# Performance work log

Hardware: AMD Instinct MI355X
Metric: run time of the kernel (lower is better)

The kernel has to match this reference:

```python
import jax, jax.numpy as jnp
import numpy as np

N, E, F_IN, HID, H, NCLS, L = 100000, 1600000, 128, 128, 4, 40, 2
C = HID // H  # per-head channels = 32
LN_EPS = 1e-5
SOFTMAX_EPS = 1e-16  # PyG softmax denominator epsilon


def setup_inputs() -> dict:
    key = jax.random.key(0)
    ks = jax.random.split(key, 8)
    s = 1.0 / np.sqrt(F_IN).astype(np.float32)
    return {
        "x": jax.random.normal(ks[0], (N, F_IN), jnp.float32),
        "edge_index": jax.random.randint(ks[1], (2, E), 0, N, jnp.int32),
        "Wq": jax.random.normal(ks[2], (L, F_IN, HID), jnp.float32) * s,
        "bq": jnp.zeros((L, HID), jnp.float32),
        "Wk": jax.random.normal(ks[3], (L, F_IN, HID), jnp.float32) * s,
        "bk": jnp.zeros((L, HID), jnp.float32),
        "Wv": jax.random.normal(ks[4], (L, F_IN, HID), jnp.float32) * s,
        "bv": jnp.zeros((L, HID), jnp.float32),
        "Ws": jax.random.normal(ks[5], (L, F_IN, HID), jnp.float32) * s,
        "bs": jnp.zeros((L, HID), jnp.float32),
        "gamma": jnp.ones((L, HID), jnp.float32),
        "beta": jnp.zeros((L, HID), jnp.float32),
        "Wout": jax.random.normal(ks[6], (HID, NCLS), jnp.float32) * (1.0 / np.sqrt(HID).astype(np.float32)),
        "bout": jnp.zeros((NCLS,), jnp.float32),
    }


def _transformer_conv(x, src, dst, Wq, bq, Wk, bk, Wv, bv, Ws, bs):
    # PyG TransformerConv, concat=False, root_weight=True, beta=False
    n = x.shape[0]
    q = (x @ Wq + bq).reshape(n, H, C)
    k = (x @ Wk + bk).reshape(n, H, C)
    v = (x @ Wv + bv).reshape(n, H, C)
    # per-edge attention logits: [E, H]
    alpha = jnp.einsum('ehc,ehc->eh', q[dst], k[src]) / np.sqrt(C).astype(np.float32)
    # segment softmax over incoming edges of each destination node
    amax = jax.ops.segment_max(alpha, dst, num_segments=n)        # [N, H]
    ex = jnp.exp(alpha - amax[dst])                               # [E, H]
    denom = jax.ops.segment_sum(ex, dst, num_segments=n)         # [N, H]
    w = ex / (denom[dst] + SOFTMAX_EPS)                           # [E, H]
    msg = v[src] * w[:, :, None]                                  # [E, H, C]
    out = jax.ops.segment_sum(msg, dst, num_segments=n)          # [N, H, C]
    out = out.mean(axis=1)                                        # concat=False -> head average, [N, C*?]. Here C*H==HID only via mean over H of C dims -> [N, C]
    # NOTE: concat=False averages heads -> [N, C]; skip proj maps in->C? In PyG, out_channels=hidden here,
    # so lin_* are Linear(in, heads*hidden)... but TransformerConv(in, hidden) means out_channels=hidden/?
    return out


def _conv(x, src, dst, Wq, bq, Wk, bk, Wv, bv, Ws, bs):
    # Faithful version with out_channels = HID per head? No: TransformerConv(in, hidden, heads, concat=False)
    # in PyG uses out_channels=hidden and lin_* : in -> heads*out_channels. To keep HID total width we model
    # per-head dim C = HID // H (standard multi-head factorization with same total width HID).
    n = x.shape[0]
    q = (x @ Wq + bq).reshape(n, H, C)
    k = (x @ Wk + bk).reshape(n, H, C)
    v = (x @ Wv + bv).reshape(n, H, C)
    alpha = jnp.einsum('ehc,ehc->eh', q[dst], k[src]) / np.sqrt(C).astype(np.float32)
    amax = jax.ops.segment_max(alpha, dst, num_segments=n)
    ex = jnp.exp(alpha - amax[dst])
    denom = jax.ops.segment_sum(ex, dst, num_segments=n)
    w = ex / (denom[dst] + SOFTMAX_EPS)
    msg = (v[src] * w[:, :, None]).reshape(-1, H * C)             # [E, HID]
    agg = jax.ops.segment_sum(msg, dst, num_segments=n)          # [N, HID]
    # concat=False -> mean over heads, then broadcast back is not what PyG does; PyG yields [N, out_channels].
    out = agg.reshape(n, H, C).mean(axis=1)                       # [N, C]
    out = jnp.tile(out, (1, H))                                   # widen back to HID? No — instead use skip of width HID.
    return out


def _conv_layer(x, src, dst, Wq, bq, Wk, bk, Wv, bv, Ws, bs):
    """TransformerConv(in, HID, heads=H, concat=False): lin_{q,k,v}: in -> H*HID is too wide for a
    memory target, so we use the equivalent standard factorization HID = H*C (per-head C), giving
    attention output [N, H, C]; concat=False head-mean is applied per head group and the result is
    projected residually via lin_skip (in -> HID)."""
    n = x.shape[0]
    q = (x @ Wq + bq).reshape(n, H, C)
    k = (x @ Wk + bk).reshape(n, H, C)
    v = (x @ Wv + bv).reshape(n, H, C)
    alpha = jnp.einsum('ehc,ehc->eh', q[dst], k[src]) / np.sqrt(C).astype(np.float32)
    amax = jax.ops.segment_max(alpha, dst, num_segments=n)        # [N, H]
    ex = jnp.exp(alpha - amax[dst])                               # [E, H]
    denom = jax.ops.segment_sum(ex, dst, num_segments=n)
    w = ex / (denom[dst] + SOFTMAX_EPS)
    msg = (v[src] * w[:, :, None]).reshape(-1, HID)               # [E, HID] (head-concat)
    agg = jax.ops.segment_sum(msg, dst, num_segments=n)          # [N, HID]
    return agg + x @ Ws + bs                                      # root/skip connection


def _layernorm(h, g, b):
    mu = h.mean(-1, keepdims=True)
    var = ((h - mu) ** 2).mean(-1, keepdims=True)
    return (h - mu) * jax.lax.rsqrt(var + LN_EPS) * g + b


def reference(x, edge_index, Wq, bq, Wk, bk, Wv, bv, Ws, bs, gamma, beta, Wout, bout):
    src, dst = edge_index[0], edge_index[1]
    h = x
    for l in range(L):  # fixed small layer count
        h = _conv_layer(h, src, dst, Wq[l], bq[l], Wk[l], bk[l], Wv[l], bv[l], Ws[l], bs[l])
        h = jax.nn.relu(_layernorm(h, gamma[l], beta[l]))
        # dropout is identity in eval mode
    return h @ Wout + bout  # [N, NCLS]
```

## Files before the change

kernel.cpp:

```cpp
#include <hip/hip_runtime.h>
#include <math.h>

#define N_NODES 100000
#define N_EDGES 1600000
#define NCLS_ 40
#define NSCAN_BLOCKS ((N_NODES + 1023) / 1024)
#define DRANGE 12500
#define SRCS_PAD (N_EDGES + 3 * N_NODES + 64)

#define QSCALE (0.17677669529663687f * 1.4426950408889634f)

#if __has_builtin(__builtin_amdgcn_exp2f)
#define EXP2(x) __builtin_amdgcn_exp2f(x)
#else
#define EXP2(x) exp2f(x)
#endif

typedef short bf16x8 __attribute__((ext_vector_type(8)));
typedef float f32x4 __attribute__((ext_vector_type(4)));

__device__ __forceinline__ unsigned short f2b(float f) {
    union { float f; unsigned u; } v; v.f = f;
    unsigned r = v.u + 0x7fffu + ((v.u >> 16) & 1u);
    return (unsigned short)(r >> 16);
}
__device__ __forceinline__ float2 up2(unsigned u) {
    union { unsigned u; float f; } a, b;
    a.u = u << 16; b.u = u & 0xffff0000u;
    return make_float2(a.f, b.f);
}
__device__ __forceinline__ unsigned pk2(float x, float y) {
    return (unsigned)f2b(x) | ((unsigned)f2b(y) << 16);
}
__device__ __forceinline__ float b2f(unsigned short s) {
    union { unsigned u; float f; } v; v.u = ((unsigned)s) << 16;
    return v.f;
}


__global__ void zero_i32_kernel(int* __restrict__ p, int n) {
    int i = blockIdx.x * blockDim.x + threadIdx.x;
    if (i < n) p[i] = 0;
}

__global__ __launch_bounds__(256) void wconv_kernel(
    const float* __restrict__ Wq, const float* __restrict__ Wk,
    const float* __restrict__ Wv, const float* __restrict__ Ws,
    unsigned short* __restrict__ Wbf) {
    int tid = blockIdx.x * 256 + threadIdx.x;
    if (tid >= 131072) return;
    int k   = tid & 127;
    int n   = (tid >> 7) & 63;
    int g   = (tid >> 13) & 1;
    int mat = (tid >> 14) & 3;
    int l   = tid >> 16;
    const float* W = (mat == 0) ? Wq : (mat == 1) ? Wk : (mat == 2) ? Wv : Ws;
    float w = W[l * 16384 + k * 128 + g * 64 + n];
    if (mat == 0) w *= QSCALE;
    Wbf[tid] = f2b(w);
}

__global__ __launch_bounds__(256) void hist_kernel(
    const int* __restrict__ dst, int* __restrict__ deg) {
    int group = blockIdx.x & 7;
    int gblk  = blockIdx.x >> 3;
    int nblk  = gridDim.x >> 3;
    int lo = group * DRANGE, hi = lo + DRANGE;
    for (int i = gblk * 256 + threadIdx.x; i < N_EDGES; i += nblk * 256) {
        int d = dst[i];
        if (d >= lo && d < hi) atomicAdd(&deg[d], 1);
    }
}

__global__ __launch_bounds__(1024) void scan_block_kernel(
    const int* __restrict__ deg, int* __restrict__ rowptr, int* __restrict__ sums) {
    __shared__ int tmp[1024];
    int t = threadIdx.x;
    int i = blockIdx.x * 1024 + t;
    int v = (i < N_NODES) ? ((deg[i] + 3) & ~3) : 0;
    tmp[t] = v;
    __syncthreads();
    for (int d = 1; d < 1024; d <<= 1) {
        int add = (t >= d) ? tmp[t - d] : 0;
        __syncthreads();
        tmp[t] += add;
        __syncthreads();
    }
    if (i < N_NODES) rowptr[i] = tmp[t] - v;
    if (t == 1023) sums[blockIdx.x] = tmp[1023];
}

__global__ __launch_bounds__(128) void scan_sums_kernel(int* __restrict__ sums) {
    __shared__ int tmp[128];
    int t = threadIdx.x;
    int v = (t < NSCAN_BLOCKS) ? sums[t] : 0;
    tmp[t] = v;
    __syncthreads();
    for (int d = 1; d < 128; d <<= 1) {
        int add = (t >= d) ? tmp[t - d] : 0;
        __syncthreads();
        tmp[t] += add;
        __syncthreads();
    }
    if (t < NSCAN_BLOCKS) sums[t] = tmp[t] - v;
}

__global__ void scan_add_kernel(int* __restrict__ rowptr, const int* __restrict__ sums,
                                int* __restrict__ cursor) {
    int i = blockIdx.x * blockDim.x + threadIdx.x;
    if (i < N_NODES) {
        int val = rowptr[i] + sums[i >> 10];
        rowptr[i] = val;
        cursor[i] = val;
    }
}

__global__ __launch_bounds__(256) void scatter_kernel(
    const int* __restrict__ src, const int* __restrict__ dst,
    int* __restrict__ cursor, int* __restrict__ srcs) {
    int group = blockIdx.x & 7;
    int gblk  = blockIdx.x >> 3;
    int nblk  = gridDim.x >> 3;
    int lo = group * DRANGE, hi = lo + DRANGE;
    for (int i = gblk * 256 + threadIdx.x; i < N_EDGES; i += nblk * 256) {
        int d = dst[i];
        if (d >= lo && d < hi) {
            int pos = atomicAdd(&cursor[d], 1);
            srcs[pos] = src[i] << 10;
        }
    }
}

__global__ __launch_bounds__(256) void gemm_qkvs_kernel(
    const void* __restrict__ Ap, int a_is_bf16,
    const unsigned short* __restrict__ Wbf,
    const float* __restrict__ b0, const float* __restrict__ b1,
    const float* __restrict__ b2, const float* __restrict__ b3,
    unsigned short* __restrict__ out) {
    __shared__ unsigned short As[64][138];
    __shared__ unsigned short Bs[2][64][138];
    int t = threadIdx.x;
    int row0 = blockIdx.x * 64;

    if (a_is_bf16) {
        const unsigned short* A = (const unsigned short*)Ap;
        for (int i = 0; i < 8; ++i) {
            int idx = t + i * 256;
            int r = idx >> 5, k4 = (idx & 31) << 2;
            ushort4 v = make_ushort4(0, 0, 0, 0);
            if (row0 + r < N_NODES) v = *(const ushort4*)&A[(size_t)(row0 + r) * 128 + k4];
            *(ushort4*)&As[r][k4] = v;
        }
    } else {
        const float* A = (const float*)Ap;
        for (int i = 0; i < 8; ++i) {
            int idx = t + i * 256;
            int r = idx >> 5, k4 = (idx & 31) << 2;
            float4 v = make_float4(0.f, 0.f, 0.f, 0.f);
            if (row0 + r < N_NODES) v = *(const float4*)&A[(size_t)(row0 + r) * 128 + k4];
            ushort4 o;
            o.x = f2b(v.x); o.y = f2b(v.y); o.z = f2b(v.z); o.w = f2b(v.w);
            *(ushort4*)&As[r][k4] = o;
        }
    }

    int wv = t >> 6, lane = t & 63;
    int ln = lane & 15, quad = lane >> 4;

    ushort4 pf[8];
    {
        const unsigned short* Wg = Wbf;
        for (int i = 0; i < 8; ++i) {
            int idx = t + i * 256;
            pf[i] = *(const ushort4*)&Wg[((idx >> 5) << 7) + ((idx & 31) << 2)];
        }
        for (int i = 0; i < 8; ++i) {
            int idx = t + i * 256;
            *(ushort4*)&Bs[0][idx >> 5][(idx & 31) << 2] = pf[i];
        }
    }
    __syncthreads();

    #pragma unroll
    for (int g = 0; g < 8; ++g) {
        int mat = g >> 1;
        int cur = g & 1;
        const float* bias = (mat == 0) ? b0 : (mat == 1) ? b1 : (mat == 2) ? b2 : b3;
        int cb = (g & 1) * 64;

        if (g < 7) {
            const unsigned short* Wg = Wbf + (size_t)(g + 1) * 8192;
            for (int i = 0; i < 8; ++i) {
                int idx = t + i * 256;
                pf[i] = *(const ushort4*)&Wg[((idx >> 5) << 7) + ((idx & 31) << 2)];
            }
        }

        f32x4 acc[4];
        for (int c = 0; c < 4; ++c) acc[c] = (f32x4){0.f, 0.f, 0.f, 0.f};
        for (int ks = 0; ks < 4; ++ks) {
            int k0 = ks * 32 + quad * 8;
            bf16x8 x = *(bf16x8*)&As[wv * 16 + ln][k0];
            for (int c = 0; c < 4; ++c) {
                bf16x8 w = *(bf16x8*)&Bs[cur][c * 16 + ln][k0];
                acc[c] = __builtin_amdgcn_mfma_f32_16x16x32_bf16(w, x, acc[c], 0, 0, 0);
            }
        }

        int node = row0 + wv * 16 + ln;
        bool ok = node < N_NODES;
        for (int c = 0; c < 4; ++c) {
            int ch = cb + c * 16 + quad * 4;
            float4 bb = *(const float4*)&bias[ch];
            float s = (mat == 0) ? QSCALE : 1.0f;
            float v0 = acc[c][0] + bb.x * s;
            float v1 = acc[c][1] + bb.y * s;
            float v2 = acc[c][2] + bb.z * s;
            float v3 = acc[c][3] + bb.w * s;
            int pos;
            if (mat == 0)      pos = ch;
            else if (mat == 3) pos = 384 + ch;
            else               pos = 128 + (ch << 1) + ((mat == 2) ? 4 : 0);
            if (ok) {
                uint2 wd;
                wd.x = pk2(v0, v1);
                wd.y = pk2(v2, v3);
                *(uint2*)&out[(size_t)node * 512 + pos] = wd;
            }
        }

        if (g < 7) {
            int nxt = cur ^ 1;
            for (int i = 0; i < 8; ++i) {
                int idx = t + i * 256;
                *(ushort4*)&Bs[nxt][idx >> 5][(idx & 31) << 2] = pf[i];
            }
        }
        __syncthreads();
    }
}

#define EDGE(KV, ECOND) {                                            \
        float2 k01 = up2(KV.x), k23 = up2(KV.y);                     \
        float p = q01.x*k01.x + q01.y*k01.y + q23.x*k23.x + q23.y*k23.y; \
        p += __shfl_xor(p, 1);                                       \
        p += __shfl_xor(p, 2);                                       \
        p += __shfl_xor(p, 4);                                       \
        float e = (ECOND);                                           \
        float2 v01 = up2(KV.z), v23 = up2(KV.w);                     \
        a0 = fmaf(e, v01.x, a0); a1 = fmaf(e, v01.y, a1);            \
        a2 = fmaf(e, v23.x, a2); a3 = fmaf(e, v23.y, a3);            \
        dsum += e; }

__global__ __launch_bounds__(256) void edge_fused_kernel(
    const unsigned short* __restrict__ qkvs,
    const int* __restrict__ srcs, const int* __restrict__ rowptr,
    const int* __restrict__ deg,
    const float* __restrict__ gamma, const float* __restrict__ beta,
    unsigned short* __restrict__ hout) {
    int n = (blockIdx.x * 256 + threadIdx.x) >> 6;
    int lane = threadIdx.x & 63;
    if (n >= N_NODES) return;
    int half = lane >> 5, hl = lane & 31;
    const unsigned short* qrow = qkvs + (size_t)n * 512;
    uint2 qu = *(const uint2*)&qrow[4 * hl];
    float2 q01 = up2(qu.x), q23 = up2(qu.y);
    uint2 su = *(const uint2*)&qrow[384 + 4 * hl];
    float2 sk01 = up2(su.x), sk23 = up2(su.y);
    int e0 = rowptr[n];
    int rem = deg[n];
    const char* kbase = (const char*)qkvs + 256 + 16 * hl;
    const int* sb = srcs + e0 + 4 * half;
    float a0 = 0.f, a1 = 0.f, a2 = 0.f, a3 = 0.f, dsum = 0.f;

    int4 oc;
    if (rem >= 8) oc = *(const int4*)sb;
    while (rem >= 8) {
        int4 on;
        if (rem >= 16) on = *(const int4*)(sb + 8);
        uint4 kv0 = *(const uint4*)(kbase + (unsigned)oc.x);
        uint4 kv1 = *(const uint4*)(kbase + (unsigned)oc.y);
        uint4 kv2 = *(const uint4*)(kbase + (unsigned)oc.z);
        uint4 kv3 = *(const uint4*)(kbase + (unsigned)oc.w);
        EDGE(kv0, EXP2(p));
        EDGE(kv1, EXP2(p));
        EDGE(kv2, EXP2(p));
        EDGE(kv3, EXP2(p));
        oc = on; sb += 8; rem -= 8;
    }
    if (rem > 0) {
        int4 ot = *(const int4*)sb;
        int tb = 4 * half;
        uint4 kv0 = *(const uint4*)(kbase + (unsigned)ot.x);
        uint4 kv1 = *(const uint4*)(kbase + (unsigned)ot.y);
        uint4 kv2 = *(const uint4*)(kbase + (unsigned)ot.z);
        uint4 kv3 = *(const uint4*)(kbase + (unsigned)ot.w);
        EDGE(kv0, (tb + 0 < rem) ? EXP2(p) : 0.f);
        EDGE(kv1, (tb + 1 < rem) ? EXP2(p) : 0.f);
        EDGE(kv2, (tb + 2 < rem) ? EXP2(p) : 0.f);
        EDGE(kv3, (tb + 3 < rem) ? EXP2(p) : 0.f);
    }

    a0 += __shfl_xor(a0, 32); a1 += __shfl_xor(a1, 32);
    a2 += __shfl_xor(a2, 32); a3 += __shfl_xor(a3, 32);
    dsum += __shfl_xor(dsum, 32);
    float dinv = 1.0f / (dsum + 1e-16f);
    float o0 = a0 * dinv + sk01.x, o1 = a1 * dinv + sk01.y;
    float o2 = a2 * dinv + sk23.x, o3 = a3 * dinv + sk23.y;
    float sum = o0 + o1 + o2 + o3;
    for (int m = 1; m < 64; m <<= 1) sum += __shfl_xor(sum, m);
    float mu = sum * (1.0f / 256.0f);
    float d0 = o0 - mu, d1 = o1 - mu, d2 = o2 - mu, d3 = o3 - mu;
    float sq = d0 * d0 + d1 * d1 + d2 * d2 + d3 * d3;
    for (int m = 1; m < 64; m <<= 1) sq += __shfl_xor(sq, m);
    float rs = rsqrtf(sq * (1.0f / 256.0f) + 1e-5f);
    if (half == 0) {
        float4 g4 = *(const float4*)&gamma[4 * hl];
        float4 b4 = *(const float4*)&beta[4 * hl];
        float r0 = fmaxf(d0 * rs * g4.x + b4.x, 0.f);
        float r1 = fmaxf(d1 * rs * g4.y + b4.y, 0.f);
        float r2 = fmaxf(d2 * rs * g4.z + b4.z, 0.f);
        float r3 = fmaxf(d3 * rs * g4.w + b4.w, 0.f);
        uint2 w;
        w.x = pk2(r0, r1);
        w.y = pk2(r2, r3);
        *(uint2*)&hout[(size_t)n * 128 + 4 * hl] = w;
    }
}

__global__ __launch_bounds__(256) void out_gemm_kernel(
    const unsigned short* __restrict__ h, const float* __restrict__ Wout,
    const float* __restrict__ bout, float* __restrict__ out) {
    int wv = __builtin_amdgcn_readfirstlane((int)(threadIdx.x >> 6));
    int l = threadIdx.x & 63;
    int n = blockIdx.x * 64 + l;
    int jb = wv * 10;
    int nc = (n < N_NODES) ? n : (N_NODES - 1);
    const unsigned short* hrow = h + (size_t)nc * 128;
    uint4 hp[16];
    #pragma unroll
    for (int i = 0; i < 16; ++i) hp[i] = *(const uint4*)&hrow[i * 8];
    float acc[10];
    #pragma unroll
    for (int j = 0; j < 10; ++j) acc[j] = bout[jb + j];
    #pragma unroll
    for (int i = 0; i < 16; ++i) {
        float2 c01 = up2(hp[i].x), c23 = up2(hp[i].y);
        float2 c45 = up2(hp[i].z), c67 = up2(hp[i].w);
        float hc0 = c01.x, hc1 = c01.y, hc2 = c23.x, hc3 = c23.y;
        float hc4 = c45.x, hc5 = c45.y, hc6 = c67.x, hc7 = c67.y;
        #pragma unroll
        for (int j = 0; j < 10; ++j) {
            const float* wk = Wout + (i * 8) * NCLS_ + jb + j;
            acc[j] = fmaf(hc0, wk[0 * NCLS_], acc[j]);
            acc[j] = fmaf(hc1, wk[1 * NCLS_], acc[j]);
            acc[j] = fmaf(hc2, wk[2 * NCLS_], acc[j]);
            acc[j] = fmaf(hc3, wk[3 * NCLS_], acc[j]);
            acc[j] = fmaf(hc4, wk[4 * NCLS_], acc[j]);
            acc[j] = fmaf(hc5, wk[5 * NCLS_], acc[j]);
            acc[j] = fmaf(hc6, wk[6 * NCLS_], acc[j]);
            acc[j] = fmaf(hc7, wk[7 * NCLS_], acc[j]);
        }
    }
    if (n < N_NODES) {
        #pragma unroll
        for (int j = 0; j < 10; ++j) out[(size_t)n * NCLS_ + jb + j] = acc[j];
    }
}

extern "C" void kernel_launch(void* const* d_in, const int* in_sizes, int n_in,
                              void* d_out, int out_size, void* d_ws, size_t ws_size,
                              hipStream_t stream) {
    const float* x    = (const float*)d_in[0];
    const int*   ei   = (const int*)d_in[1];
    const int*   src  = ei;
    const int*   dst  = ei + N_EDGES;
    const float* Wq   = (const float*)d_in[2];
    const float* bq   = (const float*)d_in[3];
    const float* Wk   = (const float*)d_in[4];
    const float* bk   = (const float*)d_in[5];
    const float* Wv   = (const float*)d_in[6];
    const float* bv   = (const float*)d_in[7];
    const float* Wsk  = (const float*)d_in[8];
    const float* bsk  = (const float*)d_in[9];
    const float* gmm  = (const float*)d_in[10];
    const float* bta  = (const float*)d_in[11];
    const float* Wout = (const float*)d_in[12];
    const float* bout = (const float*)d_in[13];
    float* outp = (float*)d_out;

    char* p = (char*)d_ws;
    auto carve = [&](size_t bytes) {
        char* r = p;
        p += (bytes + 255) & ~(size_t)255;
        return r;
    };
    unsigned short* qkvs = (unsigned short*)carve((size_t)N_NODES * 512 * 2);
    unsigned short* h    = (unsigned short*)carve((size_t)N_NODES * 128 * 2);
    unsigned short* Wbf  = (unsigned short*)carve((size_t)131072 * 2);
    int* deg     = (int*)carve((size_t)N_NODES * 4);
    int* rowptr  = (int*)carve((size_t)(N_NODES + 1) * 4);
    int* cursor  = (int*)carve((size_t)N_NODES * 4);
    int* srcs    = (int*)carve((size_t)SRCS_PAD * 4);
    int* sums    = (int*)carve((size_t)NSCAN_BLOCKS * 4);

    wconv_kernel<<<512, 256, 0, stream>>>(Wq, Wk, Wv, Wsk, Wbf);

    zero_i32_kernel<<<(N_NODES + 255) / 256, 256, 0, stream>>>(deg, N_NODES);
    zero_i32_kernel<<<(SRCS_PAD + 255) / 256, 256, 0, stream>>>(srcs, SRCS_PAD);
    hist_kernel<<<2048, 256, 0, stream>>>(dst, deg);
    scan_block_kernel<<<NSCAN_BLOCKS, 1024, 0, stream>>>(deg, rowptr, sums);
    scan_sums_kernel<<<1, 128, 0, stream>>>(sums);
    scan_add_kernel<<<(N_NODES + 255) / 256, 256, 0, stream>>>(rowptr, sums, cursor);
    scatter_kernel<<<2048, 256, 0, stream>>>(src, dst, cursor, srcs);

    for (int l = 0; l < 2; ++l) {
        const void* hin = l ? (const void*)h : (const void*)x;
        gemm_qkvs_kernel<<<(N_NODES + 63) / 64, 256, 0, stream>>>(
            hin, l, Wbf + (size_t)l * 65536,
            bq + l * 128, bk + l * 128, bv + l * 128, bsk + l * 128, qkvs);
        edge_fused_kernel<<<(N_NODES + 3) / 4, 256, 0, stream>>>(
            qkvs, srcs, rowptr, deg, gmm + l * 128, bta + l * 128, h);
    }
    out_gemm_kernel<<<(N_NODES + 63) / 64, 256, 0, stream>>>(h, Wout, bout, outp);
}
```

Before: 685.4 us.

## Load GEMM A fragments into registers, double block rows, use hardware bf16 pack

The QKVS GEMM now loads each wave's A-row fragments straight from global memory into registers instead of staging them through shared memory. Blocks grow to 512 threads covering 128 rows, so each staged weight tile is reused by twice as many rows. The software round-to-nearest bf16 packing is replaced by the v_cvt_pk_bf16_f32 instruction in the GEMM and the edge kernel. Together these aim to cut LDS traffic, weight reloads per row and conversion ALU work, at the cost of more registers per thread and reliance on the inline-asm instruction's rounding matching the old path.

```diff
diff --git a/kernel.cpp b/kernel.cpp
--- a/kernel.cpp
+++ b/kernel.cpp
@@ -24,13 +24,15 @@
     unsigned r = v.u + 0x7fffu + ((v.u >> 16) & 1u);
     return (unsigned short)(r >> 16);
 }
+__device__ __forceinline__ unsigned cvtpk(float x, float y) {
+    unsigned r;
+    asm("v_cvt_pk_bf16_f32 %0, %1, %2" : "=v"(r) : "v"(x), "v"(y));
+    return r;
+}
 __device__ __forceinline__ float2 up2(unsigned u) {
     union { unsigned u; float f; } a, b;
     a.u = u << 16; b.u = u & 0xffff0000u;
     return make_float2(a.f, b.f);
-}
-__device__ __forceinline__ unsigned pk2(float x, float y) {
-    return (unsigned)f2b(x) | ((unsigned)f2b(y) << 16);
 }
 __device__ __forceinline__ float b2f(unsigned short s) {
     union { unsigned u; float f; } v; v.u = ((unsigned)s) << 16;
@@ -131,56 +133,58 @@
     }
 }
 
-__global__ __launch_bounds__(256) void gemm_qkvs_kernel(
+__global__ __launch_bounds__(512, 4) void gemm_qkvs_kernel(
     const void* __restrict__ Ap, int a_is_bf16,
     const unsigned short* __restrict__ Wbf,
     const float* __restrict__ b0, const float* __restrict__ b1,
     const float* __restrict__ b2, const float* __restrict__ b3,
     unsigned short* __restrict__ out) {
-    __shared__ unsigned short As[64][138];
     __shared__ unsigned short Bs[2][64][138];
     int t = threadIdx.x;
-    int row0 = blockIdx.x * 64;
-
+    int row0 = blockIdx.x * 128;
+    int wr = t >> 6, lane = t & 63;
+    int ln = lane & 15, quad = lane >> 4;
+    int node = row0 + wr * 16 + ln;
+    int nodeC = (node < N_NODES) ? node : (N_NODES - 1);
+
+    bf16x8 aF[4];
     if (a_is_bf16) {
-        const unsigned short* A = (const unsigned short*)Ap;
-        for (int i = 0; i < 8; ++i) {
-            int idx = t + i * 256;
-            int r = idx >> 5, k4 = (idx & 31) << 2;
-            ushort4 v = make_ushort4(0, 0, 0, 0);
-            if (row0 + r < N_NODES) v = *(const ushort4*)&A[(size_t)(row0 + r) * 128 + k4];
-            *(ushort4*)&As[r][k4] = v;
-        }
+        const unsigned short* ar = (const unsigned short*)Ap + (size_t)nodeC * 128;
+        #pragma unroll
+        for (int ks = 0; ks < 4; ++ks)
+            aF[ks] = *(const bf16x8*)&ar[ks * 32 + quad * 8];
     } else {
-        const float* A = (const float*)Ap;
-        for (int i = 0; i < 8; ++i) {
-            int idx = t + i * 256;
-            int r = idx >> 5, k4 = (idx & 31) << 2;
-            float4 v = make_float4(0.f, 0.f, 0.f, 0.f);
-            if (row0 + r < N_NODES) v = *(const float4*)&A[(size_t)(row0 + r) * 128 + k4];
-            ushort4 o;
-            o.x = f2b(v.x); o.y = f2b(v.y); o.z = f2b(v.z); o.w = f2b(v.w);
-            *(ushort4*)&As[r][k4] = o;
-        }
-    }
-
-    int wv = t >> 6, lane = t & 63;
-    int ln = lane & 15, quad = lane >> 4;
-
-    ushort4 pf[8];
+        const float* ar = (const float*)Ap + (size_t)nodeC * 128;
+        #pragma unroll
+        for (int ks = 0; ks < 4; ++ks) {
+            float4 f0 = *(const float4*)&ar[ks * 32 + quad * 8];
+            float4 f1 = *(const float4*)&ar[ks * 32 + quad * 8 + 4];
+            union { unsigned u[4]; bf16x8 v; } cv;
+            cv.u[0] = cvtpk(f0.x, f0.y);
+            cv.u[1] = cvtpk(f0.z, f0.w);
+            cv.u[2] = cvtpk(f1.x, f1.y);
+            cv.u[3] = cvtpk(f1.z, f1.w);
+            aF[ks] = cv.v;
+        }
+    }
+
+    ushort4 pf[4];
     {
         const unsigned short* Wg = Wbf;
-        for (int i = 0; i < 8; ++i) {
-            int idx = t + i * 256;
+        #pragma unroll
+        for (int i = 0; i < 4; ++i) {
+            int idx = t + i * 512;
             pf[i] = *(const ushort4*)&Wg[((idx >> 5) << 7) + ((idx & 31) << 2)];
         }
-        for (int i = 0; i < 8; ++i) {
-            int idx = t + i * 256;
+        #pragma unroll
+        for (int i = 0; i < 4; ++i) {
+            int idx = t + i * 512;
             *(ushort4*)&Bs[0][idx >> 5][(idx & 31) << 2] = pf[i];
         }
     }
     __syncthreads();
 
+    bool ok = node < N_NODES;
     #pragma unroll
     for (int g = 0; g < 8; ++g) {
         int mat = g >> 1;
@@ -190,25 +194,27 @@
 
         if (g < 7) {
             const unsigned short* Wg = Wbf + (size_t)(g + 1) * 8192;
-            for (int i = 0; i < 8; ++i) {
-                int idx = t + i * 256;
+            #pragma unroll
+            for (int i = 0; i < 4; ++i) {
+                int idx = t + i * 512;
                 pf[i] = *(const ushort4*)&Wg[((idx >> 5) << 7) + ((idx & 31) << 2)];
             }
         }
 
         f32x4 acc[4];
+        #pragma unroll
         for (int c = 0; c < 4; ++c) acc[c] = (f32x4){0.f, 0.f, 0.f, 0.f};
+        #pragma unroll
         for (int ks = 0; ks < 4; ++ks) {
             int k0 = ks * 32 + quad * 8;
-            bf16x8 x = *(bf16x8*)&As[wv * 16 + ln][k0];
+            #pragma unroll
             for (int c = 0; c < 4; ++c) {
                 bf16x8 w = *(bf16x8*)&Bs[cur][c * 16 + ln][k0];
-                acc[c] = __builtin_amdgcn_mfma_f32_16x16x32_bf16(w, x, acc[c], 0, 0, 0);
+                acc[c] = __builtin_amdgcn_mfma_f32_16x16x32_bf16(w, aF[ks], acc[c], 0, 0, 0);
             }
         }
 
-        int node = row0 + wv * 16 + ln;
-        bool ok = node < N_NODES;
+        #pragma unroll
         for (int c = 0; c < 4; ++c) {
             int ch = cb + c * 16 + quad * 4;
             float4 bb = *(const float4*)&bias[ch];
@@ -223,16 +229,17 @@
             else               pos = 128 + (ch << 1) + ((mat == 2) ? 4 : 0);
             if (ok) {
                 uint2 wd;
-                wd.x = pk2(v0, v1);
-                wd.y = pk2(v2, v3);
+                wd.x = cvtpk(v0, v1);
+                wd.y = cvtpk(v2, v3);
                 *(uint2*)&out[(size_t)node * 512 + pos] = wd;
             }
         }
 
         if (g < 7) {
             int nxt = cur ^ 1;
-            for (int i = 0; i < 8; ++i) {
-                int idx = t + i * 256;
+            #pragma unroll
+            for (int i = 0; i < 4; ++i) {
+                int idx = t + i * 512;
                 *(ushort4*)&Bs[nxt][idx >> 5][(idx & 31) << 2] = pf[i];
             }
         }
@@ -322,8 +329,8 @@
         float r2 = fmaxf(d2 * rs * g4.z + b4.z, 0.f);
         float r3 = fmaxf(d3 * rs * g4.w + b4.w, 0.f);
         uint2 w;
-        w.x = pk2(r0, r1);
-        w.y = pk2(r2, r3);
+        w.x = cvtpk(r0, r1);
+        w.y = cvtpk(r2, r3);
         *(uint2*)&hout[(size_t)n * 128 + 4 * hl] = w;
     }
 }
@@ -416,7 +423,7 @@
 
     for (int l = 0; l < 2; ++l) {
         const void* hin = l ? (const void*)h : (const void*)x;
-        gemm_qkvs_kernel<<<(N_NODES + 63) / 64, 256, 0, stream>>>(
+        gemm_qkvs_kernel<<<(N_NODES + 127) / 128, 512, 0, stream>>>(
             hin, l, Wbf + (size_t)l * 65536,
             bq + l * 128, bk + l * 128, bv + l * 128, bsk + l * 128, qkvs);
         edge_fused_kernel<<<(N_NODES + 3) / 4, 256, 0, stream>>>(
```

Result: no change. 681.5 us (-0.6%).
